# Performance work log

Hardware: AMD Instinct MI355X
Metric: run time of the kernel (lower is better)

## Reference

```python
import jax, jax.numpy as jnp
import numpy as np

B, C, T, V, Ks = 32, 64, 64, 325, 2

def setup_inputs() -> dict:
    key = jax.random.key(0)
    k1, k2, k3, k4 = jax.random.split(key, 4)
    x = jax.random.normal(k1, (B, C, T, V), dtype=jnp.float32)
    gso = jax.random.normal(k2, (V, V), dtype=jnp.float32)
    weight = jax.random.normal(k3, (Ks, C, C), dtype=jnp.float32) * (1.0 / np.sqrt(C))
    bias = jax.random.normal(k4, (C,), dtype=jnp.float32) * 0.05
    return {"x": x, "gso": gso, "weight": weight, "bias": bias}

def reference(x, gso, weight, bias):
    # Align: c_in == c_out -> identity
    xp = jnp.transpose(x, (0, 2, 3, 1))            # [B, T, V, C]
    x1 = jnp.einsum('hi,btij->bthj', gso, xp)      # Chebyshev T1 = L @ x
    xs = jnp.stack([xp, x1], axis=2)               # [B, T, Ks, V, C]
    gc = jnp.einsum('btkhi,kij->bthj', xs, weight) + bias  # [B, T, V, C]
    out = jnp.transpose(gc, (0, 3, 1, 2)) + x      # residual, [B, C, T, V]
    return out
```

## Files before the change

kernel.cpp:

```cpp
#include <hip/hip_runtime.h>


typedef __bf16 bf16x8 __attribute__((ext_vector_type(8)));
typedef float f32x4 __attribute__((ext_vector_type(4)));

#define XROW 360
#define QROW 136
#define GROW 352

__device__ __forceinline__ float bf2f(unsigned short u) {
  union { unsigned int i; float f; } t;
  t.i = ((unsigned int)u) << 16;
  return t.f;
}
__device__ __forceinline__ unsigned short f2bf_hw(float f) {
  __bf16 b = (__bf16)f;
  union { __bf16 b; unsigned short u; } t;
  t.b = b;
  return t.u;
}

__global__ void prep_kernel(const float* __restrict__ gso,
                            const float* __restrict__ weight,
                            unsigned short* __restrict__ gso_pad,
                            unsigned short* __restrict__ wt) {
  int idx = blockIdx.x * 256 + threadIdx.x;
  if (idx < 352 * 352) {
    int v = idx / 352, u = idx - v * 352;
    unsigned short val = 0;
    if (v < 325 && u < 325) val = f2bf_hw(gso[v * 325 + u]);
    gso_pad[idx] = val;
  }
  if (idx < 2 * 64 * 64) {
    int k = idx >> 12, r = idx & 4095, c = r >> 6, i = r & 63;
    wt[idx] = f2bf_hw(weight[(k << 12) | (i << 6) | c]);
  }
}

__global__ __launch_bounds__(1024, 4) void gconv_kernel(
    const float* __restrict__ x,
    const float* __restrict__ bias,
    const unsigned short* __restrict__ gso_pad,
    const unsigned short* __restrict__ wt,
    float* __restrict__ out) {
  __shared__ unsigned short Xr[64 * XROW];
  __shared__ unsigned short XY[352 * QROW];

  const int bid = blockIdx.x;
  const int b = bid >> 6, t = bid & 63;
  const int tid = threadIdx.x;
  const int xbase = b * 1331200 + t * 325;

  {
    const int c1 = tid >> 4;
    const int u0 = tid & 15;
    const float* xrow = &x[xbase + c1 * 20800];
    unsigned short* xr = &Xr[c1 * XROW];
    unsigned short* xyc = &XY[c1];
#pragma unroll 11
    for (int k = 0; k < 22; ++k) {
      const int u = u0 + 16 * k;
      float val = (u < 325) ? xrow[u] : 0.f;
      unsigned short us = f2bf_hw(val);
      xr[u] = us;
      xyc[u * QROW] = us;
    }
  }
  __syncthreads();

  const int wid = tid >> 6, lane = tid & 63;
  const int quad = lane >> 4, l16 = lane & 15;
  const int koff = quad * 8;

  {
    const int cn = (wid & 3) * 16;
    bf16x8 bX[11];
#pragma unroll
    for (int s = 0; s < 11; ++s)
      bX[s] = *reinterpret_cast<const bf16x8*>(&Xr[(cn + l16) * XROW + s * 32 + koff]);
    for (int lt = (wid >> 2); lt < 22; lt += 4) {
      const int vb = lt * 16;
      const unsigned short* gp = &gso_pad[(vb + l16) * GROW + koff];
      f32x4 acc = {0.f, 0.f, 0.f, 0.f};
#pragma unroll
      for (int s = 0; s < 11; ++s) {
        bf16x8 ag = *reinterpret_cast<const bf16x8*>(gp + s * 32);
        acc = __builtin_amdgcn_mfma_f32_16x16x32_bf16(ag, bX[s], acc, 0, 0, 0);
      }
      const int vr = vb + quad * 4;
#pragma unroll
      for (int r = 0; r < 4; ++r)
        XY[(vr + r) * QROW + 64 + cn + l16] = f2bf_hw(acc[r]);
    }
  }
  __syncthreads();

  {
    const int cb = (wid & 3) * 16;
    bf16x8 aW[4];
#pragma unroll
    for (int s = 0; s < 4; ++s)
      aW[s] = *reinterpret_cast<const bf16x8*>(
          &wt[((s >> 1) * 64 + cb + l16) * 64 + (s & 1) * 32 + koff]);
    float bias_f[4];
#pragma unroll
    for (int r = 0; r < 4; ++r) bias_f[r] = bias[cb + quad * 4 + r];

    for (int n = (wid >> 2); n < 22; n += 4) {
      const int vb = n * 16;
      const unsigned short* xyp = &XY[(vb + l16) * QROW];
      bf16x8 bx0 = *reinterpret_cast<const bf16x8*>(xyp + koff);
      bf16x8 bx1 = *reinterpret_cast<const bf16x8*>(xyp + 32 + koff);
      bf16x8 by0 = *reinterpret_cast<const bf16x8*>(xyp + 64 + koff);
      bf16x8 by1 = *reinterpret_cast<const bf16x8*>(xyp + 96 + koff);
      f32x4 acc = {0.f, 0.f, 0.f, 0.f};
      acc = __builtin_amdgcn_mfma_f32_16x16x32_bf16(aW[0], bx0, acc, 0, 0, 0);
      acc = __builtin_amdgcn_mfma_f32_16x16x32_bf16(aW[1], bx1, acc, 0, 0, 0);
      acc = __builtin_amdgcn_mfma_f32_16x16x32_bf16(aW[2], by0, acc, 0, 0, 0);
      acc = __builtin_amdgcn_mfma_f32_16x16x32_bf16(aW[3], by1, acc, 0, 0, 0);
      const int v = vb + l16;
      if (v < 325) {
        ushort4 rx = *reinterpret_cast<const ushort4*>(xyp + cb + quad * 4);
        const unsigned short rr[4] = {rx.x, rx.y, rx.z, rx.w};
#pragma unroll
        for (int r = 0; r < 4; ++r) {
          const int c = cb + quad * 4 + r;
          out[xbase + c * 20800 + v] = acc[r] + bias_f[r] + bf2f(rr[r]);
        }
      }
    }
  }
}

extern "C" void kernel_launch(void* const* d_in, const int* in_sizes, int n_in,
                              void* d_out, int out_size, void* d_ws, size_t ws_size,
                              hipStream_t stream) {
  const float* x      = (const float*)d_in[0];
  const float* gso    = (const float*)d_in[1];
  const float* weight = (const float*)d_in[2];
  const float* bias   = (const float*)d_in[3];
  unsigned short* gso_pad = (unsigned short*)d_ws;
  unsigned short* wt      = gso_pad + 352 * 352;

  prep_kernel<<<485, 256, 0, stream>>>(gso, weight, gso_pad, wt);
  gconv_kernel<<<2048, 1024, 0, stream>>>(x, bias, gso_pad, wt, (float*)d_out);
}
```

Baseline: 436.0 us.

## Pre-swizzle gso into MFMA fragment layout and compute two channel tiles per wave

Result: faster. 385.1 us (-11.7%).

```diff
diff --git a/kernel.cpp b/kernel.cpp
--- a/kernel.cpp
+++ b/kernel.cpp
@@ -6,7 +6,7 @@
 
 #define XROW 360
 #define QROW 136
-#define GROW 352
+#define NFRAG 512
 
 __device__ __forceinline__ float bf2f(unsigned short u) {
   union { unsigned int i; float f; } t;
@@ -22,14 +22,18 @@
 
 __global__ void prep_kernel(const float* __restrict__ gso,
                             const float* __restrict__ weight,
-                            unsigned short* __restrict__ gso_pad,
+                            unsigned short* __restrict__ gfrag,
                             unsigned short* __restrict__ wt) {
   int idx = blockIdx.x * 256 + threadIdx.x;
-  if (idx < 352 * 352) {
-    int v = idx / 352, u = idx - v * 352;
+  if (idx < 22 * 11 * NFRAG) {
+    int fid = idx >> 9, r = idx & 511;
+    int l = r >> 3, j = r & 7;
+    int mt = fid / 11, s = fid - 11 * mt;
+    int v = (mt << 4) + (l & 15);
+    int u = (s << 5) + ((l >> 4) << 3) + j;
     unsigned short val = 0;
     if (v < 325 && u < 325) val = f2bf_hw(gso[v * 325 + u]);
-    gso_pad[idx] = val;
+    gfrag[idx] = val;
   }
   if (idx < 2 * 64 * 64) {
     int k = idx >> 12, r = idx & 4095, c = r >> 6, i = r & 63;
@@ -40,7 +44,7 @@
 __global__ __launch_bounds__(1024, 4) void gconv_kernel(
     const float* __restrict__ x,
     const float* __restrict__ bias,
-    const unsigned short* __restrict__ gso_pad,
+    const unsigned short* __restrict__ gfrag,
     const unsigned short* __restrict__ wt,
     float* __restrict__ out) {
   __shared__ unsigned short Xr[64 * XROW];
@@ -73,24 +77,29 @@
   const int koff = quad * 8;
 
   {
-    const int cn = (wid & 3) * 16;
-    bf16x8 bX[11];
+    const int cn = (wid & 1) * 32;
+    bf16x8 bX0[11], bX1[11];
 #pragma unroll
-    for (int s = 0; s < 11; ++s)
-      bX[s] = *reinterpret_cast<const bf16x8*>(&Xr[(cn + l16) * XROW + s * 32 + koff]);
-    for (int lt = (wid >> 2); lt < 22; lt += 4) {
-      const int vb = lt * 16;
-      const unsigned short* gp = &gso_pad[(vb + l16) * GROW + koff];
-      f32x4 acc = {0.f, 0.f, 0.f, 0.f};
+    for (int s = 0; s < 11; ++s) {
+      bX0[s] = *reinterpret_cast<const bf16x8*>(&Xr[(cn + l16) * XROW + s * 32 + koff]);
+      bX1[s] = *reinterpret_cast<const bf16x8*>(&Xr[(cn + 16 + l16) * XROW + s * 32 + koff]);
+    }
+    for (int mt = (wid >> 1); mt < 22; mt += 8) {
+      const unsigned short* gp = &gfrag[(mt * 11) * NFRAG + lane * 8];
+      f32x4 acc0 = {0.f, 0.f, 0.f, 0.f};
+      f32x4 acc1 = {0.f, 0.f, 0.f, 0.f};
 #pragma unroll
       for (int s = 0; s < 11; ++s) {
-        bf16x8 ag = *reinterpret_cast<const bf16x8*>(gp + s * 32);
-        acc = __builtin_amdgcn_mfma_f32_16x16x32_bf16(ag, bX[s], acc, 0, 0, 0);
+        bf16x8 ag = *reinterpret_cast<const bf16x8*>(gp + s * NFRAG);
+        acc0 = __builtin_amdgcn_mfma_f32_16x16x32_bf16(ag, bX0[s], acc0, 0, 0, 0);
+        acc1 = __builtin_amdgcn_mfma_f32_16x16x32_bf16(ag, bX1[s], acc1, 0, 0, 0);
       }
-      const int vr = vb + quad * 4;
+      const int vr = mt * 16 + quad * 4;
 #pragma unroll
-      for (int r = 0; r < 4; ++r)
-        XY[(vr + r) * QROW + 64 + cn + l16] = f2bf_hw(acc[r]);
+      for (int r = 0; r < 4; ++r) {
+        XY[(vr + r) * QROW + 64 + cn + l16] = f2bf_hw(acc0[r]);
+        XY[(vr + r) * QROW + 64 + cn + 16 + l16] = f2bf_hw(acc1[r]);
+      }
     }
   }
   __syncthreads();
@@ -139,9 +148,9 @@
   const float* gso    = (const float*)d_in[1];
   const float* weight = (const float*)d_in[2];
   const float* bias   = (const float*)d_in[3];
-  unsigned short* gso_pad = (unsigned short*)d_ws;
-  unsigned short* wt      = gso_pad + 352 * 352;
+  unsigned short* gfrag = (unsigned short*)d_ws;
+  unsigned short* wt    = gfrag + 22 * 11 * NFRAG;
 
-  prep_kernel<<<485, 256, 0, stream>>>(gso, weight, gso_pad, wt);
-  gconv_kernel<<<2048, 1024, 0, stream>>>(x, bias, gso_pad, wt, (float*)d_out);
+  prep_kernel<<<485, 256, 0, stream>>>(gso, weight, gfrag, wt);
+  gconv_kernel<<<2048, 1024, 0, stream>>>(x, bias, gfrag, wt, (float*)d_out);
 }
```
